# Kernel optimization log

Measured on AMD Instinct MI355X. Metric: run time of the kernel, lower is better.

## Reference

```python
import jax, jax.numpy as jnp
import numpy as np

B, L, H, E = 2, 2048, 8, 64
S = L  # self-attention


def setup_inputs() -> dict:
    key = jax.random.key(0)
    k1, k2, k3, k4, k5 = jax.random.split(key, 5)
    return {
        "queries": jax.random.normal(k1, (B, L, H, E), dtype=jnp.float32),
        "keys": jax.random.normal(k2, (B, S, H, E), dtype=jnp.float32),
        "values": jax.random.normal(k3, (B, S, H, E), dtype=jnp.float32),
        "tau": jax.random.uniform(k4, (B, 1), dtype=jnp.float32),
        "delta": jax.random.normal(k5, (B, S), dtype=jnp.float32),
    }


def reference(queries, keys, values, tau, delta):
    # De-stationary attention: scores = (QK^T) * tau + delta, causal mask, softmax, AV
    E_ = queries.shape[-1]
    scale = 1.0 / jnp.sqrt(jnp.float32(E_))
    tau_b = tau[:, None, None, :]      # [B,1,1,1]
    delta_b = delta[:, None, None, :]  # [B,1,1,S]
    scores = jnp.einsum('blhe,bshe->bhls', queries, keys) * tau_b + delta_b  # [B,H,L,S]
    Lq, Sk = scores.shape[-2], scores.shape[-1]
    causal = jnp.triu(jnp.ones((Lq, Sk), dtype=bool), k=1)  # True = masked
    scores = jnp.where(causal[None, None], -jnp.inf, scores)
    A = jax.nn.softmax(scale * scores, axis=-1)
    V = jnp.einsum('bhls,bshd->blhd', A, values)
    return V
```

## Files before the change

### kernel.cpp

```cpp
#include <hip/hip_runtime.h>


typedef _Float16 h8 __attribute__((ext_vector_type(8)));
typedef _Float16 h2 __attribute__((ext_vector_type(2)));
typedef float f32x4 __attribute__((ext_vector_type(4)));

constexpr int Bc = 2, Lc = 2048, Hc = 8, Ec = 64, Sc = 2048;
constexpr int QTL = 128;
constexpr int NQT = Lc / QTL;
constexpr int KT = 64;
constexpr int LDK = 72;
constexpr int NBH = Bc * Hc;
constexpr float SCALE = 0.125f;
constexpr float LOG2E = 1.44269504088896340736f;

__device__ __forceinline__ h2 pk2(float x, float y) {
  return __builtin_bit_cast(h2, __builtin_amdgcn_cvt_pkrtz(x, y));
}
template <int CTRL>
__device__ __forceinline__ float dpp_f(float x) {
  int r = __builtin_amdgcn_update_dpp(0, __builtin_bit_cast(int, x), CTRL, 0xF, 0xF, true);
  return __builtin_bit_cast(float, r);
}

template <int CH_IT, int EPB, int NIT>
__global__ __launch_bounds__(256, 2)
void dsattn_fwd(const float* __restrict__ Qg, const float* __restrict__ Kg,
                const float* __restrict__ Vg, const float* __restrict__ taug,
                const float* __restrict__ deltag, float* __restrict__ Og,
                _Float16* __restrict__ Opart, float* __restrict__ Lpart) {
  __shared__ __align__(16) _Float16 Ks[2][KT * LDK];
  __shared__ __align__(16) _Float16 Vt[2][Ec * LDK];
  __shared__ __align__(16) _Float16 Pb[4][16 * LDK];

  const int tid = threadIdx.x;
  const int wave = tid >> 6, lane = tid & 63;
  const int quad = lane >> 4, l16 = lane & 15;
  const int srow = tid >> 2;
  const int sec = (tid & 3) << 4;
  const int vrp = ((tid >> 3) + 4 * (tid & 7)) & 31;
  const int ve8 = (tid & 7) << 3;
  _Float16* pb = &Pb[wave][0];
  const int lo = l16 & 1;
  const int pbase = (lo ? 32 : 0) + (l16 & ~1);

  h8 onesf;
#pragma unroll
  for (int j = 0; j < 8; ++j) onesf[j] = (_Float16)1.0f;

  for (int wid = (int)blockIdx.x; wid < NIT; wid += (int)gridDim.x) {
    const int bh = wid & (NBH - 1);
    const int e = wid >> 4;
    int qt = NQT - 1, c0 = 0, pre_e = 0;
    {
      int ee = e, acc = 0;
#pragma unroll
      for (int q = NQT - 1; q >= 0; --q) {
        const int n = (2 * q + 1 + CH_IT) / CH_IT;
        if (ee < n) { qt = q; c0 = ee; pre_e = EPB - acc - n; break; }
        ee -= n; acc += n;
      }
    }
    const int ntiles = 2 * qt + 2;
    const int nch = (ntiles + CH_IT - 1) / CH_IT;
    const int ktBeg = c0 * CH_IT;
    const int ktEnd = min(ktBeg + CH_IT - 1, ntiles - 1);
    const int q0 = qt * QTL;
    const int b = bh >> 3, h = bh & 7;
    const float ct = taug[b] * (SCALE * LOG2E);

    h8 qfrag[2][2];
#pragma unroll
    for (int f = 0; f < 2; ++f)
#pragma unroll
      for (int kk = 0; kk < 2; ++kk) {
        const float* qp = Qg + (((size_t)b * Lc + q0 + 32 * wave + 16 * f + l16) * Hc + h) * Ec
                         + quad * 8 + kk * 32;
        const float4* p = (const float4*)qp;
        union { h8 v; h2 c[4]; } u;
        float4 a0 = p[0], a1 = p[1];
        u.c[0] = pk2(a0.x, a0.y); u.c[1] = pk2(a0.z, a0.w);
        u.c[2] = pk2(a1.x, a1.y); u.c[3] = pk2(a1.z, a1.w);
        qfrag[f][kk] = u.v;
      }

    f32x4 Oacc[2][4], Osum[2];
#pragma unroll
    for (int f = 0; f < 2; ++f) {
#pragma unroll
      for (int nt = 0; nt < 4; ++nt) Oacc[f][nt] = (f32x4){0.f, 0.f, 0.f, 0.f};
      Osum[f] = (f32x4){0.f, 0.f, 0.f, 0.f};
    }

    float dcur[4];

    __syncthreads();

    {
      const int kb = ktBeg * KT;
      const float* kp = Kg + (((size_t)b * Sc + kb + srow) * Hc + h) * Ec + sec;
      float4 c0v = ((const float4*)kp)[0], c1v = ((const float4*)kp)[1];
      float4 c2v = ((const float4*)kp)[2], c3v = ((const float4*)kp)[3];
      const float* vp0 = Vg + (((size_t)b * Sc + kb + 2 * vrp) * Hc + h) * Ec + ve8;
      const float* vp1 = vp0 + Hc * Ec;
      float4 r00 = ((const float4*)vp0)[0], r01 = ((const float4*)vp0)[1];
      float4 r10 = ((const float4*)vp1)[0], r11 = ((const float4*)vp1)[1];
#pragma unroll
      for (int nt = 0; nt < 4; ++nt)
        dcur[nt] = deltag[(size_t)b * Sc + kb + nt * 16 + l16] * (SCALE * LOG2E);
      union { h8 v; h2 c[4]; } w0, w1;
      w0.c[0] = pk2(c0v.x, c0v.y); w0.c[1] = pk2(c0v.z, c0v.w);
      w0.c[2] = pk2(c1v.x, c1v.y); w0.c[3] = pk2(c1v.z, c1v.w);
      w1.c[0] = pk2(c2v.x, c2v.y); w1.c[1] = pk2(c2v.z, c2v.w);
      w1.c[2] = pk2(c3v.x, c3v.y); w1.c[3] = pk2(c3v.z, c3v.w);
      *(h8*)&Ks[0][srow * LDK + sec] = w0.v;
      *(h8*)&Ks[0][srow * LDK + sec + 8] = w1.v;
      const float e0[8] = {r00.x, r00.y, r00.z, r00.w, r01.x, r01.y, r01.z, r01.w};
      const float e1[8] = {r10.x, r10.y, r10.z, r10.w, r11.x, r11.y, r11.z, r11.w};
#pragma unroll
      for (int j = 0; j < 8; ++j)
        *(h2*)&Vt[0][(ve8 + j) * LDK + 2 * vrp] = pk2(e0[j], e1[j]);
    }

    for (int kt = ktBeg; kt <= ktEnd; ++kt) {
      const int cur = (kt - ktBeg) & 1;
      const bool pf = (kt < ktEnd);
      const int kbase = kt * KT;

      __syncthreads();

      float4 kn0, kn1, kn2, kn3, vn00, vn01, vn10, vn11;
      float dn[4];
      if (pf) {
        const int nb = (kt + 1) * KT;
        const float* kp = Kg + (((size_t)b * Sc + nb + srow) * Hc + h) * Ec + sec;
        kn0 = ((const float4*)kp)[0]; kn1 = ((const float4*)kp)[1];
        kn2 = ((const float4*)kp)[2]; kn3 = ((const float4*)kp)[3];
        const float* vp0 = Vg + (((size_t)b * Sc + nb + 2 * vrp) * Hc + h) * Ec + ve8;
        const float* vp1 = vp0 + Hc * Ec;
        vn00 = ((const float4*)vp0)[0]; vn01 = ((const float4*)vp0)[1];
        vn10 = ((const float4*)vp1)[0]; vn11 = ((const float4*)vp1)[1];
#pragma unroll
        for (int nt = 0; nt < 4; ++nt)
          dn[nt] = deltag[(size_t)b * Sc + nb + nt * 16 + l16];
      }

      const int wtop = q0 + 32 * wave + 31;
      if (kbase <= wtop) {
        f32x4 Sacc[2][4];
#pragma unroll
        for (int f = 0; f < 2; ++f)
#pragma unroll
          for (int nt = 0; nt < 4; ++nt) Sacc[f][nt] = (f32x4){0.f, 0.f, 0.f, 0.f};
#pragma unroll
        for (int kk = 0; kk < 2; ++kk) {
          h8 bf[4];
#pragma unroll
          for (int nt = 0; nt < 4; ++nt)
            bf[nt] = *(const h8*)&Ks[cur][(nt * 16 + l16) * LDK + quad * 8 + kk * 32];
#pragma unroll
          for (int f = 0; f < 2; ++f)
#pragma unroll
            for (int nt = 0; nt < 4; ++nt)
              Sacc[f][nt] = __builtin_amdgcn_mfma_f32_16x16x32_f16(qfrag[f][kk], bf[nt], Sacc[f][nt], 0, 0, 0);
        }

#pragma unroll
        for (int f = 0; f < 2; ++f) {
          const int fr0 = q0 + 32 * wave + 16 * f;
          float sv[4][4];
#pragma unroll
          for (int nt = 0; nt < 4; ++nt)
#pragma unroll
            for (int r = 0; r < 4; ++r)
              sv[nt][r] = Sacc[f][nt][r] * ct + dcur[nt];
          if (kbase + 63 > fr0) {
#pragma unroll
            for (int nt = 0; nt < 4; ++nt) {
              const int key = kbase + nt * 16 + l16;
#pragma unroll
              for (int r = 0; r < 4; ++r)
                if (key > fr0 + quad * 4 + r) sv[nt][r] = -1e30f;
            }
          }
#pragma unroll
          for (int nt = 0; nt < 4; ++nt)
#pragma unroll
            for (int r = 0; r < 4; ++r)
              sv[nt][r] = __builtin_amdgcn_exp2f(sv[nt][r]);

#pragma unroll
          for (int r = 0; r < 4; ++r) {
            float o0 = dpp_f<0xB1>(sv[0][r]);
            float o1 = dpp_f<0xB1>(sv[1][r]);
            float o2 = dpp_f<0xB1>(sv[2][r]);
            float o3 = dpp_f<0xB1>(sv[3][r]);
            h2 d0 = lo ? pk2(o2, sv[2][r]) : pk2(sv[0][r], o0);
            h2 d1 = lo ? pk2(o3, sv[3][r]) : pk2(sv[1][r], o1);
            _Float16* pp = &pb[((quad << 2) + r) * LDK + pbase];
            *(h2*)pp = d0;
            *(h2*)(pp + 16) = d1;
          }
          asm volatile("s_waitcnt lgkmcnt(0)" ::: "memory");

          h8 af0 = *(const h8*)&pb[l16 * LDK + quad * 8];
          h8 af1 = *(const h8*)&pb[l16 * LDK + quad * 8 + 32];

#pragma unroll
          for (int nt = 0; nt < 4; ++nt) {
            h8 vf0 = *(const h8*)&Vt[cur][(nt * 16 + l16) * LDK + quad * 8];
            Oacc[f][nt] = __builtin_amdgcn_mfma_f32_16x16x32_f16(af0, vf0, Oacc[f][nt], 0, 0, 0);
            h8 vf1 = *(const h8*)&Vt[cur][(nt * 16 + l16) * LDK + quad * 8 + 32];
            Oacc[f][nt] = __builtin_amdgcn_mfma_f32_16x16x32_f16(af1, vf1, Oacc[f][nt], 0, 0, 0);
          }
          Osum[f] = __builtin_amdgcn_mfma_f32_16x16x32_f16(af0, onesf, Osum[f], 0, 0, 0);
          Osum[f] = __builtin_amdgcn_mfma_f32_16x16x32_f16(af1, onesf, Osum[f], 0, 0, 0);
        }
      }

      if (pf) {
        _Float16* ksn = &Ks[cur ^ 1][0];
        _Float16* vtn = &Vt[cur ^ 1][0];
        union { h8 v; h2 c[4]; } w0, w1;
        w0.c[0] = pk2(kn0.x, kn0.y); w0.c[1] = pk2(kn0.z, kn0.w);
        w0.c[2] = pk2(kn1.x, kn1.y); w0.c[3] = pk2(kn1.z, kn1.w);
        w1.c[0] = pk2(kn2.x, kn2.y); w1.c[1] = pk2(kn2.z, kn2.w);
        w1.c[2] = pk2(kn3.x, kn3.y); w1.c[3] = pk2(kn3.z, kn3.w);
        *(h8*)&ksn[srow * LDK + sec] = w0.v;
        *(h8*)&ksn[srow * LDK + sec + 8] = w1.v;
        const float e0[8] = {vn00.x, vn00.y, vn00.z, vn00.w, vn01.x, vn01.y, vn01.z, vn01.w};
        const float e1[8] = {vn10.x, vn10.y, vn10.z, vn10.w, vn11.x, vn11.y, vn11.z, vn11.w};
#pragma unroll
        for (int j = 0; j < 8; ++j)
          *(h2*)&vtn[(ve8 + j) * LDK + 2 * vrp] = pk2(e0[j], e1[j]);
#pragma unroll
        for (int nt = 0; nt < 4; ++nt) dcur[nt] = dn[nt] * (SCALE * LOG2E);
      }
    }

    if (nch == 1) {
#pragma unroll
      for (int f = 0; f < 2; ++f)
#pragma unroll
        for (int r = 0; r < 4; ++r) {
          const int qrow = q0 + 32 * wave + 16 * f + (quad << 2) + r;
          const float inv = 1.0f / Osum[f][r];
          float* op = Og + (((size_t)b * Lc + qrow) * Hc + h) * Ec;
#pragma unroll
          for (int nt = 0; nt < 4; ++nt) op[nt * 16 + l16] = Oacc[f][nt][r] * inv;
        }
    } else {
      const int en = bh * EPB + pre_e + c0;
      _Float16* op = Opart + (size_t)en * (QTL * Ec);
#pragma unroll
      for (int f = 0; f < 2; ++f)
#pragma unroll
        for (int r = 0; r < 4; ++r) {
          const int row = 32 * wave + 16 * f + (quad << 2) + r;
#pragma unroll
          for (int nt = 0; nt < 4; ++nt)
            op[row * Ec + nt * 16 + l16] = (_Float16)Oacc[f][nt][r];
          if (l16 == 0) Lpart[en * QTL + row] = Osum[f][r];
        }
    }
  }
}

template <int CH_IT, int EPB>
__global__ __launch_bounds__(256, 4)
void dsattn_comb(const _Float16* __restrict__ Opart, const float* __restrict__ Lpart,
                 float* __restrict__ Og) {
  const int qt = (CH_IT / 2) + ((int)blockIdx.x >> 2);
  const int slab = (int)blockIdx.x & 3;
  const int bh = (int)blockIdx.y;
  const int b = bh >> 3, h = bh & 7;
  const int nch = (2 * qt + 1 + CH_IT) / CH_IT;
  int pre_e = 0;
#pragma unroll
  for (int q = 0; q < NQT; ++q)
    if (q < qt) pre_e += (2 * q + 1 + CH_IT) / CH_IT;
  const int e0 = bh * EPB + pre_e;

  const int row = slab * 32 + ((int)threadIdx.x >> 3);
  const int col = ((int)threadIdx.x & 7) << 3;

  float acc[8];
#pragma unroll
  for (int i = 0; i < 8; ++i) acc[i] = 0.f;
  float l = 0.f;
  for (int c = 0; c < nch; ++c) {
    l += Lpart[(e0 + c) * QTL + row];
    h8 v = *(const h8*)(Opart + (size_t)(e0 + c) * (QTL * Ec) + row * Ec + col);
#pragma unroll
    for (int i = 0; i < 8; ++i) acc[i] += (float)v[i];
  }
  const float inv = 1.0f / l;
  float* out = Og + (((size_t)b * Lc + qt * QTL + row) * Hc + h) * Ec + col;
  float4 o0, o1;
  o0.x = acc[0] * inv; o0.y = acc[1] * inv; o0.z = acc[2] * inv; o0.w = acc[3] * inv;
  o1.x = acc[4] * inv; o1.y = acc[5] * inv; o1.z = acc[6] * inv; o1.w = acc[7] * inv;
  ((float4*)out)[0] = o0;
  ((float4*)out)[1] = o1;
}

extern "C" void kernel_launch(void* const* d_in, const int* in_sizes, int n_in,
                              void* d_out, int out_size, void* d_ws, size_t ws_size,
                              hipStream_t stream) {
  const float* Q = (const float*)d_in[0];
  const float* K = (const float*)d_in[1];
  const float* V = (const float*)d_in[2];
  const float* tau = (const float*)d_in[3];
  const float* delta = (const float*)d_in[4];
  float* O = (float*)d_out;

  constexpr int CH = 4;
  constexpr int EPB = 72;
  constexpr int TOT_E = Bc * Hc * EPB;
  constexpr int PERS = 768;
  const size_t need = (size_t)TOT_E * QTL * Ec * 2 + (size_t)TOT_E * QTL * 4;

  if (ws_size >= need) {
    _Float16* Opart = (_Float16*)d_ws;
    float* Lpart = (float*)(Opart + (size_t)TOT_E * QTL * Ec);
    dsattn_fwd<CH, EPB, TOT_E><<<dim3(PERS), 256, 0, stream>>>(
        Q, K, V, tau, delta, O, Opart, Lpart);
    dim3 g2((NQT - CH / 2) * 4, Bc * Hc);
    dsattn_comb<CH, EPB><<<g2, 256, 0, stream>>>(Opart, Lpart, O);
  } else {
    dsattn_fwd<32, NQT, NQT * NBH><<<dim3(NQT * NBH), 256, 0, stream>>>(
        Q, K, V, tau, delta, O, nullptr, nullptr);
  }
}
```

Measured before the change: 109.7 us.

## Pre-convert K to fp16 in a prep kernel and load MFMA fragments directly

A new prep kernel converts K to a per-head fp16 layout in workspace. The attention kernel then loads K fragments straight from global memory into registers, dropping the K shared-memory tile and its conversion work. The P buffer is widened so both row groups are staged before a single PV pass that reuses each V fragment across two MFMAs. This adds an extra launch and an extra round trip through global memory for K. In the fallback path, Kh is written to workspace without checking that the workspace is large enough.

```diff
diff --git a/kernel.cpp b/kernel.cpp
--- a/kernel.cpp
+++ b/kernel.cpp
@@ -23,21 +23,38 @@
   return __builtin_bit_cast(float, r);
 }
 
+__global__ __launch_bounds__(256)
+void dsattn_prep(const float* __restrict__ Kg, _Float16* __restrict__ Kh) {
+  const int bh = (int)blockIdx.y;
+  const int b = bh >> 3, h = bh & 7;
+  const int s0 = (int)blockIdx.x * 64;
+  const int tid = (int)threadIdx.x;
+  const int srow = tid >> 2, sec = (tid & 3) << 4;
+  const float* kp = Kg + (((size_t)b * Sc + s0 + srow) * Hc + h) * Ec + sec;
+  float4 c0 = ((const float4*)kp)[0], c1 = ((const float4*)kp)[1];
+  float4 c2 = ((const float4*)kp)[2], c3 = ((const float4*)kp)[3];
+  union { h8 v; h2 c[4]; } w0, w1;
+  w0.c[0] = pk2(c0.x, c0.y); w0.c[1] = pk2(c0.z, c0.w);
+  w0.c[2] = pk2(c1.x, c1.y); w0.c[3] = pk2(c1.z, c1.w);
+  w1.c[0] = pk2(c2.x, c2.y); w1.c[1] = pk2(c2.z, c2.w);
+  w1.c[2] = pk2(c3.x, c3.y); w1.c[3] = pk2(c3.z, c3.w);
+  _Float16* ko = Kh + ((size_t)bh * Sc + s0 + srow) * Ec + sec;
+  *(h8*)ko = w0.v;
+  *(h8*)(ko + 8) = w1.v;
+}
+
 template <int CH_IT, int EPB, int NIT>
 __global__ __launch_bounds__(256, 2)
-void dsattn_fwd(const float* __restrict__ Qg, const float* __restrict__ Kg,
+void dsattn_fwd(const float* __restrict__ Qg, const _Float16* __restrict__ Kh,
                 const float* __restrict__ Vg, const float* __restrict__ taug,
                 const float* __restrict__ deltag, float* __restrict__ Og,
                 _Float16* __restrict__ Opart, float* __restrict__ Lpart) {
-  __shared__ __align__(16) _Float16 Ks[2][KT * LDK];
   __shared__ __align__(16) _Float16 Vt[2][Ec * LDK];
-  __shared__ __align__(16) _Float16 Pb[4][16 * LDK];
+  __shared__ __align__(16) _Float16 Pb[4][32 * LDK];
 
   const int tid = threadIdx.x;
   const int wave = tid >> 6, lane = tid & 63;
   const int quad = lane >> 4, l16 = lane & 15;
-  const int srow = tid >> 2;
-  const int sec = (tid & 3) << 4;
   const int vrp = ((tid >> 3) + 4 * (tid & 7)) & 31;
   const int ve8 = (tid & 7) << 3;
   _Float16* pb = &Pb[wave][0];
@@ -68,6 +85,7 @@
     const int q0 = qt * QTL;
     const int b = bh >> 3, h = bh & 7;
     const float ct = taug[b] * (SCALE * LOG2E);
+    const _Float16* kbh = Kh + (size_t)bh * Sc * Ec;
 
     h8 qfrag[2][2];
 #pragma unroll
@@ -93,14 +111,17 @@
     }
 
     float dcur[4];
+    h8 kf[4][2];
 
     __syncthreads();
 
     {
       const int kb = ktBeg * KT;
-      const float* kp = Kg + (((size_t)b * Sc + kb + srow) * Hc + h) * Ec + sec;
-      float4 c0v = ((const float4*)kp)[0], c1v = ((const float4*)kp)[1];
-      float4 c2v = ((const float4*)kp)[2], c3v = ((const float4*)kp)[3];
+#pragma unroll
+      for (int nt = 0; nt < 4; ++nt)
+#pragma unroll
+        for (int kk = 0; kk < 2; ++kk)
+          kf[nt][kk] = *(const h8*)&kbh[(size_t)(kb + nt * 16 + l16) * Ec + quad * 8 + kk * 32];
       const float* vp0 = Vg + (((size_t)b * Sc + kb + 2 * vrp) * Hc + h) * Ec + ve8;
       const float* vp1 = vp0 + Hc * Ec;
       float4 r00 = ((const float4*)vp0)[0], r01 = ((const float4*)vp0)[1];
@@ -108,13 +129,6 @@
 #pragma unroll
       for (int nt = 0; nt < 4; ++nt)
         dcur[nt] = deltag[(size_t)b * Sc + kb + nt * 16 + l16] * (SCALE * LOG2E);
-      union { h8 v; h2 c[4]; } w0, w1;
-      w0.c[0] = pk2(c0v.x, c0v.y); w0.c[1] = pk2(c0v.z, c0v.w);
-      w0.c[2] = pk2(c1v.x, c1v.y); w0.c[3] = pk2(c1v.z, c1v.w);
-      w1.c[0] = pk2(c2v.x, c2v.y); w1.c[1] = pk2(c2v.z, c2v.w);
-      w1.c[2] = pk2(c3v.x, c3v.y); w1.c[3] = pk2(c3v.z, c3v.w);
-      *(h8*)&Ks[0][srow * LDK + sec] = w0.v;
-      *(h8*)&Ks[0][srow * LDK + sec + 8] = w1.v;
       const float e0[8] = {r00.x, r00.y, r00.z, r00.w, r01.x, r01.y, r01.z, r01.w};
       const float e1[8] = {r10.x, r10.y, r10.z, r10.w, r11.x, r11.y, r11.z, r11.w};
 #pragma unroll
@@ -129,13 +143,16 @@
 
       __syncthreads();
 
-      float4 kn0, kn1, kn2, kn3, vn00, vn01, vn10, vn11;
+      float4 vn00, vn01, vn10, vn11;
       float dn[4];
+      h8 kfn[4][2];
       if (pf) {
         const int nb = (kt + 1) * KT;
-        const float* kp = Kg + (((size_t)b * Sc + nb + srow) * Hc + h) * Ec + sec;
-        kn0 = ((const float4*)kp)[0]; kn1 = ((const float4*)kp)[1];
-        kn2 = ((const float4*)kp)[2]; kn3 = ((const float4*)kp)[3];
+#pragma unroll
+        for (int nt = 0; nt < 4; ++nt)
+#pragma unroll
+          for (int kk = 0; kk < 2; ++kk)
+            kfn[nt][kk] = *(const h8*)&kbh[(size_t)(nb + nt * 16 + l16) * Ec + quad * 8 + kk * 32];
         const float* vp0 = Vg + (((size_t)b * Sc + nb + 2 * vrp) * Hc + h) * Ec + ve8;
         const float* vp1 = vp0 + Hc * Ec;
         vn00 = ((const float4*)vp0)[0]; vn01 = ((const float4*)vp0)[1];
@@ -153,17 +170,12 @@
 #pragma unroll
           for (int nt = 0; nt < 4; ++nt) Sacc[f][nt] = (f32x4){0.f, 0.f, 0.f, 0.f};
 #pragma unroll
-        for (int kk = 0; kk < 2; ++kk) {
-          h8 bf[4];
-#pragma unroll
-          for (int nt = 0; nt < 4; ++nt)
-            bf[nt] = *(const h8*)&Ks[cur][(nt * 16 + l16) * LDK + quad * 8 + kk * 32];
+        for (int kk = 0; kk < 2; ++kk)
 #pragma unroll
           for (int f = 0; f < 2; ++f)
 #pragma unroll
             for (int nt = 0; nt < 4; ++nt)
-              Sacc[f][nt] = __builtin_amdgcn_mfma_f32_16x16x32_f16(qfrag[f][kk], bf[nt], Sacc[f][nt], 0, 0, 0);
-        }
+              Sacc[f][nt] = __builtin_amdgcn_mfma_f32_16x16x32_f16(qfrag[f][kk], kf[nt][kk], Sacc[f][nt], 0, 0, 0);
 
 #pragma unroll
         for (int f = 0; f < 2; ++f) {
@@ -188,7 +200,6 @@
 #pragma unroll
             for (int r = 0; r < 4; ++r)
               sv[nt][r] = __builtin_amdgcn_exp2f(sv[nt][r]);
-
 #pragma unroll
           for (int r = 0; r < 4; ++r) {
             float o0 = dpp_f<0xB1>(sv[0][r]);
@@ -197,44 +208,48 @@
             float o3 = dpp_f<0xB1>(sv[3][r]);
             h2 d0 = lo ? pk2(o2, sv[2][r]) : pk2(sv[0][r], o0);
             h2 d1 = lo ? pk2(o3, sv[3][r]) : pk2(sv[1][r], o1);
-            _Float16* pp = &pb[((quad << 2) + r) * LDK + pbase];
+            _Float16* pp = &pb[(16 * f + (quad << 2) + r) * LDK + pbase];
             *(h2*)pp = d0;
             *(h2*)(pp + 16) = d1;
           }
-          asm volatile("s_waitcnt lgkmcnt(0)" ::: "memory");
-
-          h8 af0 = *(const h8*)&pb[l16 * LDK + quad * 8];
-          h8 af1 = *(const h8*)&pb[l16 * LDK + quad * 8 + 32];
-
+        }
+        asm volatile("s_waitcnt lgkmcnt(0)" ::: "memory");
+
+        h8 af[2][2];
+#pragma unroll
+        for (int f = 0; f < 2; ++f)
+#pragma unroll
+          for (int kk = 0; kk < 2; ++kk)
+            af[f][kk] = *(const h8*)&pb[(16 * f + l16) * LDK + quad * 8 + kk * 32];
+
+#pragma unroll
+        for (int kk = 0; kk < 2; ++kk) {
 #pragma unroll
           for (int nt = 0; nt < 4; ++nt) {
-            h8 vf0 = *(const h8*)&Vt[cur][(nt * 16 + l16) * LDK + quad * 8];
-            Oacc[f][nt] = __builtin_amdgcn_mfma_f32_16x16x32_f16(af0, vf0, Oacc[f][nt], 0, 0, 0);
-            h8 vf1 = *(const h8*)&Vt[cur][(nt * 16 + l16) * LDK + quad * 8 + 32];
-            Oacc[f][nt] = __builtin_amdgcn_mfma_f32_16x16x32_f16(af1, vf1, Oacc[f][nt], 0, 0, 0);
+            h8 vf = *(const h8*)&Vt[cur][(nt * 16 + l16) * LDK + quad * 8 + kk * 32];
+#pragma unroll
+            for (int f = 0; f < 2; ++f)
+              Oacc[f][nt] = __builtin_amdgcn_mfma_f32_16x16x32_f16(af[f][kk], vf, Oacc[f][nt], 0, 0, 0);
           }
-          Osum[f] = __builtin_amdgcn_mfma_f32_16x16x32_f16(af0, onesf, Osum[f], 0, 0, 0);
-          Osum[f] = __builtin_amdgcn_mfma_f32_16x16x32_f16(af1, onesf, Osum[f], 0, 0, 0);
+#pragma unroll
+          for (int f = 0; f < 2; ++f)
+            Osum[f] = __builtin_amdgcn_mfma_f32_16x16x32_f16(af[f][kk], onesf, Osum[f], 0, 0, 0);
         }
       }
 
       if (pf) {
-        _Float16* ksn = &Ks[cur ^ 1][0];
         _Float16* vtn = &Vt[cur ^ 1][0];
-        union { h8 v; h2 c[4]; } w0, w1;
-        w0.c[0] = pk2(kn0.x, kn0.y); w0.c[1] = pk2(kn0.z, kn0.w);
-        w0.c[2] = pk2(kn1.x, kn1.y); w0.c[3] = pk2(kn1.z, kn1.w);
-        w1.c[0] = pk2(kn2.x, kn2.y); w1.c[1] = pk2(kn2.z, kn2.w);
-        w1.c[2] = pk2(kn3.x, kn3.y); w1.c[3] = pk2(kn3.z, kn3.w);
-        *(h8*)&ksn[srow * LDK + sec] = w0.v;
-        *(h8*)&ksn[srow * LDK + sec + 8] = w1.v;
         const float e0[8] = {vn00.x, vn00.y, vn00.z, vn00.w, vn01.x, vn01.y, vn01.z, vn01.w};
         const float e1[8] = {vn10.x, vn10.y, vn10.z, vn10.w, vn11.x, vn11.y, vn11.z, vn11.w};
 #pragma unroll
         for (int j = 0; j < 8; ++j)
           *(h2*)&vtn[(ve8 + j) * LDK + 2 * vrp] = pk2(e0[j], e1[j]);
 #pragma unroll
-        for (int nt = 0; nt < 4; ++nt) dcur[nt] = dn[nt] * (SCALE * LOG2E);
+        for (int nt = 0; nt < 4; ++nt) {
+          dcur[nt] = dn[nt] * (SCALE * LOG2E);
+#pragma unroll
+          for (int kk = 0; kk < 2; ++kk) kf[nt][kk] = kfn[nt][kk];
+        }
       }
     }
 
@@ -317,17 +332,23 @@
   constexpr int EPB = 72;
   constexpr int TOT_E = Bc * Hc * EPB;
   constexpr int PERS = 768;
-  const size_t need = (size_t)TOT_E * QTL * Ec * 2 + (size_t)TOT_E * QTL * 4;
+  constexpr size_t KVH = (size_t)NBH * Sc * Ec;
+
+  _Float16* Kh = (_Float16*)d_ws;
+  _Float16* Opart = Kh + KVH;
+  float* Lpart = (float*)(Opart + (size_t)TOT_E * QTL * Ec);
+  const size_t need = KVH * 2 + (size_t)TOT_E * QTL * Ec * 2
+                    + (size_t)TOT_E * QTL * 4;
+
+  dsattn_prep<<<dim3(Sc / 64, NBH), 256, 0, stream>>>(K, Kh);
 
   if (ws_size >= need) {
-    _Float16* Opart = (_Float16*)d_ws;
-    float* Lpart = (float*)(Opart + (size_t)TOT_E * QTL * Ec);
     dsattn_fwd<CH, EPB, TOT_E><<<dim3(PERS), 256, 0, stream>>>(
-        Q, K, V, tau, delta, O, Opart, Lpart);
+        Q, Kh, V, tau, delta, O, Opart, Lpart);
     dim3 g2((NQT - CH / 2) * 4, Bc * Hc);
     dsattn_comb<CH, EPB><<<g2, 256, 0, stream>>>(Opart, Lpart, O);
   } else {
     dsattn_fwd<32, NQT, NQT * NBH><<<dim3(NQT * NBH), 256, 0, stream>>>(
-        Q, K, V, tau, delta, O, nullptr, nullptr);
+        Q, Kh, V, tau, delta, O, nullptr, nullptr);
   }
 }
```

Measured after the change: 118.4 us. 8.0% more time.
